# Performance work log

Measured on AMD Instinct MI355X. Metric: run time of the kernel, lower is better.

Reference implementation:

```python
import jax, jax.numpy as jnp
import numpy as np


def _bitlinear(x, w_latent):
    # per-output-row abs-mean scale, ternary round with straight-through estimator
    scale = jax.lax.stop_gradient(
        jnp.clip(jnp.mean(jnp.abs(w_latent), axis=1, keepdims=True), 1e-5, None))
    tern = jnp.clip(jnp.round(w_latent / scale), -1.0, 1.0)
    w = w_latent + jax.lax.stop_gradient(tern - w_latent)  # STE
    return x @ (w * scale).T


def setup_inputs() -> dict:
    key = jax.random.key(0)
    ks = jax.random.split(key, 6)
    dim, hidden, rank = 1024, 4096, 16
    B, S = 4, 4096
    x = jax.random.normal(ks[0], (B, S, dim), dtype=jnp.float32)
    w_fc = 0.02 * jax.random.normal(ks[1], (hidden, dim), dtype=jnp.float32)
    w_proj = 0.02 * jax.random.normal(ks[2], (dim, hidden), dtype=jnp.float32)
    u = 0.02 * jax.random.normal(ks[3], (hidden, rank), dtype=jnp.float32)
    v = 0.02 * jax.random.normal(ks[4], (rank, dim), dtype=jnp.float32)
    fast_b = jax.random.normal(ks[5], (rank, rank), dtype=jnp.float32)
    gate = jnp.float32(0.05)
    return {"x": x, "fast_b": fast_b, "w_fc": w_fc, "w_proj": w_proj,
            "u": u, "v": v, "gate": gate}


def reference(x, fast_b, w_fc, w_proj, u, v, gate):
    # fc BitLinear + low-rank fast adapter delta
    h = _bitlinear(x, w_fc) + gate * (((x @ v.T) @ fast_b.T) @ u.T)
    r = jnp.maximum(h, 0.0)
    return _bitlinear(r * r, w_proj)  # ReLU^2 then proj BitLinear
```

## Files before the change

### kernel.cpp

```cpp
#include <hip/hip_runtime.h>


typedef unsigned short u16;
typedef __attribute__((ext_vector_type(8))) short short8;
typedef __attribute__((ext_vector_type(4))) float float4v;

#define M_TOK   16384
#define DIM     1024
#define HID     4096


__device__ __forceinline__ u16 f2bf(float f) {
    union { float f; unsigned u; } v; v.f = f;
    unsigned r = v.u + 0x7fffu + ((v.u >> 16) & 1u);
    return (u16)(r >> 16);
}

__device__ __forceinline__ void gload_lds16(const u16* g, u16* l) {
    __builtin_amdgcn_global_load_lds(
        (const __attribute__((address_space(1))) void*)g,
        (__attribute__((address_space(3))) void*)l, 16, 0, 0);
}


__global__ __launch_bounds__(256) void cvt_x_kernel(const float* __restrict__ x,
                                                    u16* __restrict__ y) {
    int i = (blockIdx.x * 256 + threadIdx.x) * 4;
    float4 v = *reinterpret_cast<const float4*>(x + i);
    ushort4 o;
    o.x = f2bf(v.x); o.y = f2bf(v.y); o.z = f2bf(v.z); o.w = f2bf(v.w);
    *reinterpret_cast<ushort4*>(y + i) = o;
}

__global__ __launch_bounds__(256) void adapter_T_kernel(const float* __restrict__ u,
                                                        const float* __restrict__ fb,
                                                        float* __restrict__ T) {
    int i = blockIdx.x * 256 + threadIdx.x;
    int row = i >> 4, r = i & 15;
    float s = 0.f;
#pragma unroll
    for (int k = 0; k < 16; k++) s += u[row * 16 + k] * fb[k * 16 + r];
    T[i] = s;
}

__global__ __launch_bounds__(256) void build_w1_kernel(const float* __restrict__ w,
                                                       const float* __restrict__ T,
                                                       const float* __restrict__ v,
                                                       const float* __restrict__ gate,
                                                       u16* __restrict__ W1) {
    const int row = blockIdx.x, tid = threadIdx.x;
    float s = 0.f;
#pragma unroll
    for (int jj = 0; jj < 4; jj++) s += fabsf(w[row * 1024 + tid + jj * 256]);
#pragma unroll
    for (int o = 32; o > 0; o >>= 1) s += __shfl_down(s, o, 64);
    __shared__ float red[4];
    if ((tid & 63) == 0) red[tid >> 6] = s;
    __syncthreads();
    const float scale = fmaxf((red[0] + red[1] + red[2] + red[3]) * (1.f / 1024.f), 1e-5f);
    const float g = gate[0];
    float t[16];
#pragma unroll
    for (int r = 0; r < 16; r++) t[r] = T[row * 16 + r];
#pragma unroll
    for (int jj = 0; jj < 4; jj++) {
        const int j = tid + jj * 256;
        const float wv = w[row * 1024 + j];
        float tern = rintf(wv / scale);
        tern = fminf(1.f, fmaxf(-1.f, tern));
        float ad = 0.f;
#pragma unroll
        for (int r = 0; r < 16; r++) ad += t[r] * v[r * 1024 + j];
        W1[row * 1024 + j] = f2bf(tern * scale + g * ad);
    }
}

__global__ __launch_bounds__(256) void build_w2_kernel(const float* __restrict__ w,
                                                       u16* __restrict__ W2) {
    const int row = blockIdx.x, tid = threadIdx.x;
    float s = 0.f;
#pragma unroll
    for (int jj = 0; jj < 16; jj++) s += fabsf(w[row * 4096 + tid + jj * 256]);
#pragma unroll
    for (int o = 32; o > 0; o >>= 1) s += __shfl_down(s, o, 64);
    __shared__ float red[4];
    if ((tid & 63) == 0) red[tid >> 6] = s;
    __syncthreads();
    const float scale = fmaxf((red[0] + red[1] + red[2] + red[3]) * (1.f / 4096.f), 1e-5f);
#pragma unroll
    for (int jj = 0; jj < 16; jj++) {
        const int j = tid + jj * 256;
        float tern = rintf(w[row * 4096 + j] / scale);
        tern = fminf(1.f, fmaxf(-1.f, tern));
        W2[row * 4096 + j] = f2bf(tern * scale);
    }
}

template <int N, int K, int EPI>
__global__ __launch_bounds__(256, 2) void gemm_bt(const u16* __restrict__ A,
                                                  const u16* __restrict__ B,
                                                  void* __restrict__ Cv) {
    __shared__ alignas(16) u16 As[128 * 64];
    __shared__ alignas(16) u16 Bs[128 * 64];
    const int tid = threadIdx.x;
    const int bn = blockIdx.x, bm = blockIdx.y;
    const int wave = tid >> 6, lane = tid & 63;
    const int wm = (wave >> 1) << 6;
    const int wn = (wave & 1) << 6;
    const int lr = lane & 15, quad = lane >> 4;

    float4v acc[4][4];
#pragma unroll
    for (int i = 0; i < 4; i++)
#pragma unroll
        for (int j = 0; j < 4; j++) acc[i][j] = (float4v)0.0f;

    const u16* Ag[4];
    const u16* Bg[4];
    u16* Al[4];
    u16* Bl[4];
#pragma unroll
    for (int c = 0; c < 4; c++) {
        const int q = tid + c * 256;
        const int row = q >> 3, p = q & 7;
        const int kc = p ^ (row & 7);
        Ag[c] = A + (size_t)(bm * 128 + row) * K + kc * 8;
        Bg[c] = B + (size_t)(bn * 128 + row) * K + kc * 8;
        Al[c] = As + q * 8;
        Bl[c] = Bs + q * 8;
    }

    int offA[4][2], offB[4][2];
#pragma unroll
    for (int i = 0; i < 4; i++)
#pragma unroll
        for (int ks = 0; ks < 2; ks++) {
            const int p = ((4 * ks + quad) ^ (lr & 7)) * 8;
            offA[i][ks] = (wm + lr + 16 * i) * 64 + p;
            offB[i][ks] = (wn + lr + 16 * i) * 64 + p;
        }

    for (int k0 = 0; k0 < K; k0 += 64) {
#pragma unroll
        for (int c = 0; c < 4; c++) gload_lds16(Ag[c] + k0, Al[c]);
#pragma unroll
        for (int c = 0; c < 4; c++) gload_lds16(Bg[c] + k0, Bl[c]);
        __syncthreads();
#pragma unroll
        for (int ks = 0; ks < 2; ks++) {
            short8 af[4], bfr[4];
#pragma unroll
            for (int i = 0; i < 4; i++)
                af[i] = *reinterpret_cast<const short8*>(As + offA[i][ks]);
#pragma unroll
            for (int j = 0; j < 4; j++)
                bfr[j] = *reinterpret_cast<const short8*>(Bs + offB[j][ks]);
#pragma unroll
            for (int i = 0; i < 4; i++)
#pragma unroll
                for (int j = 0; j < 4; j++)
                    acc[i][j] = __builtin_amdgcn_mfma_f32_16x16x32_bf16(
                        af[i], bfr[j], acc[i][j], 0, 0, 0);
        }
        __syncthreads();
    }

    const int row0 = bm * 128 + wm + quad * 4;
    const int col0 = bn * 128 + wn + lr;
#pragma unroll
    for (int i = 0; i < 4; i++)
#pragma unroll
        for (int j = 0; j < 4; j++) {
            const int col = col0 + j * 16;
#pragma unroll
            for (int r = 0; r < 4; r++) {
                const int row = row0 + i * 16 + r;
                const float vv = acc[i][j][r];
                if (EPI == 0) {
                    const float rr = fmaxf(vv, 0.f);
                    ((u16*)Cv)[(size_t)row * N + col] = f2bf(rr * rr);
                } else {
                    ((float*)Cv)[(size_t)row * N + col] = vv;
                }
            }
        }
}


extern "C" void kernel_launch(void* const* d_in, const int* in_sizes, int n_in,
                              void* d_out, int out_size, void* d_ws, size_t ws_size,
                              hipStream_t stream) {
    const float* x      = (const float*)d_in[0];
    const float* fast_b = (const float*)d_in[1];
    const float* w_fc   = (const float*)d_in[2];
    const float* w_proj = (const float*)d_in[3];
    const float* u      = (const float*)d_in[4];
    const float* v      = (const float*)d_in[5];
    const float* gate   = (const float*)d_in[6];
    float* out = (float*)d_out;

    char* ws = (char*)d_ws;
    u16*   Xb  = (u16*)(ws + 0);
    u16*   W1  = (u16*)(ws + 33554432);
    u16*   W2  = (u16*)(ws + 41943040);
    u16*   RSQ = (u16*)(ws + 50331648);
    float* T   = (float*)(ws + 184549376);

    cvt_x_kernel<<<M_TOK * DIM / (256 * 4), 256, 0, stream>>>(x, Xb);
    adapter_T_kernel<<<HID * 16 / 256, 256, 0, stream>>>(u, fast_b, T);
    build_w1_kernel<<<HID, 256, 0, stream>>>(w_fc, T, v, gate, W1);
    build_w2_kernel<<<DIM, 256, 0, stream>>>(w_proj, W2);

    gemm_bt<HID, DIM, 0><<<dim3(HID / 128, M_TOK / 128), 256, 0, stream>>>(Xb, W1, RSQ);
    gemm_bt<DIM, HID, 1><<<dim3(DIM / 128, M_TOK / 128), 256, 0, stream>>>(RSQ, W2, out);
}
```

Baseline: 463.9 us.

## Rewrite GEMM as 256x256 tile, 8-wave, double-buffered pipelined kernel

Replaces the 128x128 single-buffered GEMM with a 256x256 tile kernel using 512 threads and double-buffered LDS. Global-to-LDS loads for tile t+2 are issued during compute, using explicit vmcnt waits, barriers and setprio around the MFMA phases. It also adds an XCD-aware block remapping to improve L2 locality. The aim is to hide load latency and cut LDS/global traffic per FLOP, at the cost of more registers and 128KB of LDS, which limits occupancy.

```diff
diff --git a/kernel.cpp b/kernel.cpp
--- a/kernel.cpp
+++ b/kernel.cpp
@@ -97,93 +97,193 @@
 }
 
 template <int N, int K, int EPI>
-__global__ __launch_bounds__(256, 2) void gemm_bt(const u16* __restrict__ A,
+__global__ __launch_bounds__(512, 2) void gemm256(const u16* __restrict__ A,
                                                   const u16* __restrict__ B,
                                                   void* __restrict__ Cv) {
-    __shared__ alignas(16) u16 As[128 * 64];
-    __shared__ alignas(16) u16 Bs[128 * 64];
-    const int tid = threadIdx.x;
-    const int bn = blockIdx.x, bm = blockIdx.y;
+    constexpr int GM  = M_TOK / 256;
+    constexpr int GN  = N / 256;
+    constexpr int NWG = GM * GN;
+    constexpr int NT  = K / 64;
+
+    __shared__ alignas(16) u16 lds[2][2][256 * 64];
+
+    const int tid  = threadIdx.x;
     const int wave = tid >> 6, lane = tid & 63;
-    const int wm = (wave >> 1) << 6;
-    const int wn = (wave & 1) << 6;
     const int lr = lane & 15, quad = lane >> 4;
-
-    float4v acc[4][4];
-#pragma unroll
-    for (int i = 0; i < 4; i++)
-#pragma unroll
-        for (int j = 0; j < 4; j++) acc[i][j] = (float4v)0.0f;
-
-    const u16* Ag[4];
-    const u16* Bg[4];
-    u16* Al[4];
-    u16* Bl[4];
+    const int wm = (wave >> 2) << 7;
+    const int wn = (wave & 3) << 6;
+
+    int flat = (int)blockIdx.x;
+    flat = (flat & 7) * (NWG / 8) + (flat >> 3);
+    const int bm = flat % GM;
+    const int bn = flat / GM;
+
+    const u16* Ag[4]; const u16* Bg[4]; int qo[4];
 #pragma unroll
     for (int c = 0; c < 4; c++) {
-        const int q = tid + c * 256;
+        const int q = tid + c * 512;
         const int row = q >> 3, p = q & 7;
         const int kc = p ^ (row & 7);
-        Ag[c] = A + (size_t)(bm * 128 + row) * K + kc * 8;
-        Bg[c] = B + (size_t)(bn * 128 + row) * K + kc * 8;
-        Al[c] = As + q * 8;
-        Bl[c] = Bs + q * 8;
+        Ag[c] = A + (size_t)(bm * 256 + row) * K + kc * 8;
+        Bg[c] = B + (size_t)(bn * 256 + row) * K + kc * 8;
+        qo[c] = q * 8;
     }
 
-    int offA[4][2], offB[4][2];
-#pragma unroll
-    for (int i = 0; i < 4; i++)
-#pragma unroll
-        for (int ks = 0; ks < 2; ks++) {
-            const int p = ((4 * ks + quad) ^ (lr & 7)) * 8;
-            offA[i][ks] = (wm + lr + 16 * i) * 64 + p;
-            offB[i][ks] = (wn + lr + 16 * i) * 64 + p;
-        }
-
-    for (int k0 = 0; k0 < K; k0 += 64) {
-#pragma unroll
-        for (int c = 0; c < 4; c++) gload_lds16(Ag[c] + k0, Al[c]);
-#pragma unroll
-        for (int c = 0; c < 4; c++) gload_lds16(Bg[c] + k0, Bl[c]);
-        __syncthreads();
-#pragma unroll
-        for (int ks = 0; ks < 2; ks++) {
-            short8 af[4], bfr[4];
-#pragma unroll
-            for (int i = 0; i < 4; i++)
-                af[i] = *reinterpret_cast<const short8*>(As + offA[i][ks]);
-#pragma unroll
-            for (int j = 0; j < 4; j++)
-                bfr[j] = *reinterpret_cast<const short8*>(Bs + offB[j][ks]);
-#pragma unroll
-            for (int i = 0; i < 4; i++)
-#pragma unroll
-                for (int j = 0; j < 4; j++)
+    float4v acc[8][4];
+#pragma unroll
+    for (int i = 0; i < 8; i++)
+#pragma unroll
+        for (int j = 0; j < 4; j++) acc[i][j] = (float4v)0.0f;
+
+    const int pk0 = (quad ^ (lr & 7)) * 8;
+    const int pk1 = ((4 + quad) ^ (lr & 7)) * 8;
+
+#define STAGE(buf, k0)                                                        \
+    do {                                                                      \
+        u16* la_ = &lds[buf][0][0]; u16* lb_ = &lds[buf][1][0];               \
+        _Pragma("unroll")                                                     \
+        for (int c_ = 0; c_ < 4; c_++) gload_lds16(Ag[c_] + (k0), la_ + qo[c_]); \
+        _Pragma("unroll")                                                     \
+        for (int c_ = 0; c_ < 4; c_++) gload_lds16(Bg[c_] + (k0), lb_ + qo[c_]); \
+    } while (0)
+
+#define BAR()                                                                 \
+    do {                                                                      \
+        __builtin_amdgcn_sched_barrier(0);                                    \
+        __builtin_amdgcn_s_barrier();                                         \
+        __builtin_amdgcn_sched_barrier(0);                                    \
+    } while (0)
+
+    STAGE(0, 0);
+    STAGE(1, 64);
+    __builtin_amdgcn_sched_barrier(0);
+    asm volatile("s_waitcnt vmcnt(8)" ::: "memory");
+    __builtin_amdgcn_s_barrier();
+    __builtin_amdgcn_sched_barrier(0);
+    asm volatile("" ::: "memory");
+
+    for (int t = 0; t < NT; ++t) {
+        const int cur = t & 1;
+        const u16* Ab = &lds[cur][0][0];
+        const u16* Bb = &lds[cur][1][0];
+        short8 af[4][2], b0[2][2], b1[2][2];
+
+#pragma unroll
+        for (int i = 0; i < 4; i++) {
+            const u16* rp = Ab + (wm + i * 16 + lr) * 64;
+            af[i][0] = *reinterpret_cast<const short8*>(rp + pk0);
+            af[i][1] = *reinterpret_cast<const short8*>(rp + pk1);
+        }
+#pragma unroll
+        for (int j = 0; j < 2; j++) {
+            const u16* rp = Bb + (wn + j * 16 + lr) * 64;
+            b0[j][0] = *reinterpret_cast<const short8*>(rp + pk0);
+            b0[j][1] = *reinterpret_cast<const short8*>(rp + pk1);
+        }
+        BAR();
+        __builtin_amdgcn_s_setprio(1);
+#pragma unroll
+        for (int i = 0; i < 4; i++)
+#pragma unroll
+            for (int j = 0; j < 2; j++)
+#pragma unroll
+                for (int ks = 0; ks < 2; ks++)
                     acc[i][j] = __builtin_amdgcn_mfma_f32_16x16x32_bf16(
-                        af[i], bfr[j], acc[i][j], 0, 0, 0);
-        }
-        __syncthreads();
+                        af[i][ks], b0[j][ks], acc[i][j], 0, 0, 0);
+        __builtin_amdgcn_s_setprio(0);
+        BAR();
+
+#pragma unroll
+        for (int j = 0; j < 2; j++) {
+            const u16* rp = Bb + (wn + 32 + j * 16 + lr) * 64;
+            b1[j][0] = *reinterpret_cast<const short8*>(rp + pk0);
+            b1[j][1] = *reinterpret_cast<const short8*>(rp + pk1);
+        }
+        BAR();
+        __builtin_amdgcn_s_setprio(1);
+#pragma unroll
+        for (int i = 0; i < 4; i++)
+#pragma unroll
+            for (int j = 0; j < 2; j++)
+#pragma unroll
+                for (int ks = 0; ks < 2; ks++)
+                    acc[i][2 + j] = __builtin_amdgcn_mfma_f32_16x16x32_bf16(
+                        af[i][ks], b1[j][ks], acc[i][2 + j], 0, 0, 0);
+        __builtin_amdgcn_s_setprio(0);
+        BAR();
+
+#pragma unroll
+        for (int i = 0; i < 4; i++) {
+            const u16* rp = Ab + (wm + 64 + i * 16 + lr) * 64;
+            af[i][0] = *reinterpret_cast<const short8*>(rp + pk0);
+            af[i][1] = *reinterpret_cast<const short8*>(rp + pk1);
+        }
+        BAR();
+        __builtin_amdgcn_s_setprio(1);
+#pragma unroll
+        for (int i = 0; i < 4; i++)
+#pragma unroll
+            for (int j = 0; j < 2; j++)
+#pragma unroll
+                for (int ks = 0; ks < 2; ks++)
+                    acc[4 + i][j] = __builtin_amdgcn_mfma_f32_16x16x32_bf16(
+                        af[i][ks], b0[j][ks], acc[4 + i][j], 0, 0, 0);
+        __builtin_amdgcn_s_setprio(0);
+        BAR();
+
+        asm volatile("" ::: "memory");
+        if (t + 2 < NT) {
+            STAGE(cur, (t + 2) * 64);
+        }
+        __builtin_amdgcn_sched_barrier(0);
+        __builtin_amdgcn_s_setprio(1);
+#pragma unroll
+        for (int i = 0; i < 4; i++)
+#pragma unroll
+            for (int j = 0; j < 2; j++)
+#pragma unroll
+                for (int ks = 0; ks < 2; ks++)
+                    acc[4 + i][2 + j] = __builtin_amdgcn_mfma_f32_16x16x32_bf16(
+                        af[i][ks], b1[j][ks], acc[4 + i][2 + j], 0, 0, 0);
+        __builtin_amdgcn_s_setprio(0);
+        __builtin_amdgcn_sched_barrier(0);
+        if (t + 1 < NT) {
+            if (t + 2 < NT) {
+                asm volatile("s_waitcnt vmcnt(8)" ::: "memory");
+            } else {
+                asm volatile("s_waitcnt vmcnt(0)" ::: "memory");
+            }
+            __builtin_amdgcn_s_barrier();
+            __builtin_amdgcn_sched_barrier(0);
+            asm volatile("" ::: "memory");
+        }
     }
-
-    const int row0 = bm * 128 + wm + quad * 4;
-    const int col0 = bn * 128 + wn + lr;
-#pragma unroll
-    for (int i = 0; i < 4; i++)
-#pragma unroll
-        for (int j = 0; j < 4; j++) {
-            const int col = col0 + j * 16;
-#pragma unroll
-            for (int r = 0; r < 4; r++) {
-                const int row = row0 + i * 16 + r;
-                const float vv = acc[i][j][r];
-                if (EPI == 0) {
-                    const float rr = fmaxf(vv, 0.f);
-                    ((u16*)Cv)[(size_t)row * N + col] = f2bf(rr * rr);
-                } else {
-                    ((float*)Cv)[(size_t)row * N + col] = vv;
+#undef STAGE
+#undef BAR
+
+    const int row0 = bm * 256 + wm + quad * 4;
+    const int col0 = bn * 256 + wn + lr;
+#pragma unroll
+    for (int qr = 0; qr < 2; qr++)
+#pragma unroll
+        for (int i = 0; i < 4; i++)
+#pragma unroll
+            for (int qc = 0; qc < 2; qc++)
+#pragma unroll
+                for (int j = 0; j < 2; j++) {
+                    const int col = col0 + qc * 32 + j * 16;
+                    const float4v a = acc[qr * 4 + i][qc * 2 + j];
+#pragma unroll
+                    for (int r = 0; r < 4; r++) {
+                        const int row = row0 + qr * 64 + i * 16 + r;
+                        if (EPI == 0) {
+                            const float rr = fmaxf(a[r], 0.f);
+                            ((u16*)Cv)[(size_t)row * N + col] = f2bf(rr * rr);
+                        } else {
+                            ((float*)Cv)[(size_t)row * N + col] = a[r];
+                        }
+                    }
                 }
-            }
-        }
 }
 
 
@@ -211,6 +311,6 @@
     build_w1_kernel<<<HID, 256, 0, stream>>>(w_fc, T, v, gate, W1);
     build_w2_kernel<<<DIM, 256, 0, stream>>>(w_proj, W2);
 
-    gemm_bt<HID, DIM, 0><<<dim3(HID / 128, M_TOK / 128), 256, 0, stream>>>(Xb, W1, RSQ);
-    gemm_bt<DIM, HID, 1><<<dim3(DIM / 128, M_TOK / 128), 256, 0, stream>>>(RSQ, W2, out);
-}
+    gemm256<HID, DIM, 0><<<dim3((M_TOK / 256) * (HID / 256)), 512, 0, stream>>>(Xb, W1, RSQ);
+    gemm256<DIM, HID, 1><<<dim3((M_TOK / 256) * (DIM / 256)), 512, 0, stream>>>(RSQ, W2, out);
+}
```

After: 415.2 us. -10.5%, faster.
